# Performance work log

Measured on AMD Instinct MI355X. Metric: run time of the kernel, lower is better.

Reference implementation:

```python
import jax, jax.numpy as jnp
import numpy as np

NUM_ENTITIES = 600
FIRST_ENTITY = 0
LAST_ENTITY = 511  # inclusive, as in attentions[:, first:last+1]
EPS = 1e-9


def setup_inputs() -> dict:
    key = jax.random.key(0)
    k1, k2, k3, k4 = jax.random.split(key, 4)
    B, S, E = 64, 4096, 128
    doc_emb = jax.random.normal(k1, (B, S, E), dtype=jnp.float32)
    query_emb = jax.random.normal(k2, (B, E), dtype=jnp.float32)
    doc_ids = jax.random.randint(k3, (B, S), 0, NUM_ENTITIES, dtype=jnp.int32)
    seq_length = jax.random.randint(k4, (B,), 0, S, dtype=jnp.int32)
    return {"doc_emb": doc_emb, "query_emb": query_emb,
            "doc_ids": doc_ids, "seq_length": seq_length}


def reference(doc_emb, query_emb, doc_ids, seq_length):
    B, S, E = doc_emb.shape
    # --- _calculate_attention: batched mat-vec + length-masked softmax ---
    scores = jnp.einsum('bse,be->bs', doc_emb, query_emb)          # [B,S]
    seq_len = jnp.maximum(seq_length, 1)                            # guard empty docs
    valid = jnp.arange(S)[None, :] < seq_len[:, None]               # [B,S] bool
    scores = jnp.where(valid, scores, jnp.float32(-1e30))
    attentions = jax.nn.softmax(scores, axis=-1)                    # [B,S]
    # --- _sum_attentions: per-batch unsorted_segment_sum over entity ids ---
    # offset trick replaces tf.map_fn-serialized segment sums with one batched scatter
    seg_ids = (doc_ids + jnp.arange(B, dtype=doc_ids.dtype)[:, None] * NUM_ENTITIES).reshape(-1)
    sums = jax.ops.segment_sum(attentions.reshape(-1), seg_ids,
                               num_segments=B * NUM_ENTITIES)
    sums = sums.reshape(B, NUM_ENTITIES)[:, FIRST_ENTITY:LAST_ENTITY + 1]  # [B,512]
    # --- softmax_inverse: log (eps for numerical safety on zero-mass entities) ---
    logits = jnp.log(sums + EPS)
    return logits
```

## Files before the change

kernel.cpp:

```cpp
#include <hip/hip_runtime.h>
#include <hip/hip_bf16.h>
#include <math.h>

#define BB 64
#define SS 4096
#define EE 128
#define NENT 600
#define NOUT 512

__global__ __launch_bounds__(256) void scores_kernel(
    const float* __restrict__ doc_emb,
    const float* __restrict__ query_emb,
    float* __restrict__ scores) {
  const int b     = blockIdx.y;
  const int chunk = blockIdx.x;
  const int tid   = threadIdx.x;
  const int wave  = tid >> 6;
  const int lane  = tid & 63;
  const int half  = lane >> 5;
  const int sub   = lane & 31;

  const float4 q = ((const float4*)(query_emb + b * EE))[sub];

  const float* base = doc_emb + (size_t)b * SS * EE;
  const int s0 = chunk * 128 + wave * 2 + half;

#pragma unroll
  for (int it = 0; it < 16; ++it) {
    const int s = s0 + it * 8;
    const float4 d = ((const float4*)(base + (size_t)s * EE))[sub];
    float p = d.x * q.x + d.y * q.y + d.z * q.z + d.w * q.w;
#pragma unroll
    for (int off = 16; off; off >>= 1) p += __shfl_down(p, off, 32);
    if (sub == 0) scores[b * SS + s] = p;
  }
}

__global__ __launch_bounds__(1024) void finish_kernel(
    const float* __restrict__ scores,
    const int* __restrict__ doc_ids,
    const int* __restrict__ seq_length,
    float* __restrict__ out) {
  const int b   = blockIdx.x;
  const int tid = threadIdx.x;
  const int lane = tid & 63;
  const int wv   = tid >> 6;

  int len = seq_length[b];
  if (len < 1) len = 1;

  __shared__ float red[16];
  __shared__ float s_max, s_sum;
  __shared__ float bins[NENT];

  const float* sc = scores + b * SS;

  float vals[4];
  float lmax = -1e30f;
#pragma unroll
  for (int i = 0; i < 4; ++i) {
    const int s = tid + i * 1024;
    const float v = (s < len) ? sc[s] : -1e30f;
    vals[i] = v;
    lmax = fmaxf(lmax, v);
  }
#pragma unroll
  for (int off = 32; off; off >>= 1) lmax = fmaxf(lmax, __shfl_down(lmax, off, 64));
  if (lane == 0) red[wv] = lmax;
  __syncthreads();
  if (tid < 16) {
    float m = red[tid];
#pragma unroll
    for (int off = 8; off; off >>= 1) m = fmaxf(m, __shfl_down(m, off, 16));
    if (tid == 0) s_max = m;
  }
  __syncthreads();
  const float mx = s_max;
  __syncthreads();

  float lsum = 0.f;
#pragma unroll
  for (int i = 0; i < 4; ++i) {
    const int s = tid + i * 1024;
    const float e = (s < len) ? expf(vals[i] - mx) : 0.f;
    vals[i] = e;
    lsum += e;
  }
#pragma unroll
  for (int off = 32; off; off >>= 1) lsum += __shfl_down(lsum, off, 64);
  if (lane == 0) red[wv] = lsum;
  __syncthreads();
  if (tid < 16) {
    float m = red[tid];
#pragma unroll
    for (int off = 8; off; off >>= 1) m += __shfl_down(m, off, 16);
    if (tid == 0) s_sum = m;
  }
  for (int i = tid; i < NENT; i += 1024) bins[i] = 0.f;
  __syncthreads();
  const float inv = 1.f / s_sum;

  const int* ids = doc_ids + b * SS;
#pragma unroll
  for (int i = 0; i < 4; ++i) {
    const int s = tid + i * 1024;
    if (s < len) atomicAdd(&bins[ids[s]], vals[i] * inv);
  }
  __syncthreads();

  if (tid < NOUT) out[b * NOUT + tid] = logf(bins[tid] + 1e-9f);
}

extern "C" void kernel_launch(void* const* d_in, const int* in_sizes, int n_in,
                              void* d_out, int out_size, void* d_ws, size_t ws_size,
                              hipStream_t stream) {
  const float* doc_emb    = (const float*)d_in[0];
  const float* query_emb  = (const float*)d_in[1];
  const int*   doc_ids    = (const int*)d_in[2];
  const int*   seq_length = (const int*)d_in[3];
  float* out    = (float*)d_out;
  float* scores = (float*)d_ws;

  dim3 grid1(SS / 128, BB);
  scores_kernel<<<grid1, 256, 0, stream>>>(doc_emb, query_emb, scores);
  finish_kernel<<<BB, 1024, 0, stream>>>(scores, doc_ids, seq_length, out);
}
```

Baseline: 202.7 us.

## Fuse scoring, exponentiation and segment-sum via global atomics without max subtraction

Folds the softmax and segment-sum into the score kernel. Each score is exponentiated directly, with no max subtraction, and atomically added into global per-entity bins and a per-batch denominator. A small finalize kernel then normalizes and takes the log. This removes the scores round-trip and the single-block-per-batch finish kernel, but adds a memset, global atomic contention, and a risk of overflow or precision loss because exp is taken without the max shift.

```diff
diff --git a/kernel.cpp b/kernel.cpp
--- a/kernel.cpp
+++ b/kernel.cpp
@@ -8,10 +8,13 @@
 #define NENT 600
 #define NOUT 512
 
-__global__ __launch_bounds__(256) void scores_kernel(
+__global__ __launch_bounds__(256) void fused_kernel(
     const float* __restrict__ doc_emb,
     const float* __restrict__ query_emb,
-    float* __restrict__ scores) {
+    const int* __restrict__ doc_ids,
+    const int* __restrict__ seq_length,
+    float* __restrict__ bins,
+    float* __restrict__ denom) {
   const int b     = blockIdx.y;
   const int chunk = blockIdx.x;
   const int tid   = threadIdx.x;
@@ -20,10 +23,16 @@
   const int half  = lane >> 5;
   const int sub   = lane & 31;
 
+  int len = seq_length[b];
+  if (len < 1) len = 1;
+
   const float4 q = ((const float4*)(query_emb + b * EE))[sub];
+  const float* base = doc_emb + (size_t)b * SS * EE;
+  const int* ids = doc_ids + b * SS;
+  float* mybins = bins + b * NENT;
 
-  const float* base = doc_emb + (size_t)b * SS * EE;
   const int s0 = chunk * 128 + wave * 2 + half;
+  float dsum = 0.f;
 
 #pragma unroll
   for (int it = 0; it < 16; ++it) {
@@ -32,83 +41,24 @@
     float p = d.x * q.x + d.y * q.y + d.z * q.z + d.w * q.w;
 #pragma unroll
     for (int off = 16; off; off >>= 1) p += __shfl_down(p, off, 32);
-    if (sub == 0) scores[b * SS + s] = p;
+    if (sub == 0 && s < len) {
+      const float e = __expf(p);
+      atomicAdd(&mybins[ids[s]], e);
+      dsum += e;
+    }
   }
+  dsum += __shfl_down(dsum, 32, 64);
+  if (lane == 0 && dsum > 0.f) atomicAdd(&denom[b], dsum);
 }
 
-__global__ __launch_bounds__(1024) void finish_kernel(
-    const float* __restrict__ scores,
-    const int* __restrict__ doc_ids,
-    const int* __restrict__ seq_length,
+__global__ __launch_bounds__(512) void finalize_kernel(
+    const float* __restrict__ bins,
+    const float* __restrict__ denom,
     float* __restrict__ out) {
-  const int b   = blockIdx.x;
-  const int tid = threadIdx.x;
-  const int lane = tid & 63;
-  const int wv   = tid >> 6;
-
-  int len = seq_length[b];
-  if (len < 1) len = 1;
-
-  __shared__ float red[16];
-  __shared__ float s_max, s_sum;
-  __shared__ float bins[NENT];
-
-  const float* sc = scores + b * SS;
-
-  float vals[4];
-  float lmax = -1e30f;
-#pragma unroll
-  for (int i = 0; i < 4; ++i) {
-    const int s = tid + i * 1024;
-    const float v = (s < len) ? sc[s] : -1e30f;
-    vals[i] = v;
-    lmax = fmaxf(lmax, v);
-  }
-#pragma unroll
-  for (int off = 32; off; off >>= 1) lmax = fmaxf(lmax, __shfl_down(lmax, off, 64));
-  if (lane == 0) red[wv] = lmax;
-  __syncthreads();
-  if (tid < 16) {
-    float m = red[tid];
-#pragma unroll
-    for (int off = 8; off; off >>= 1) m = fmaxf(m, __shfl_down(m, off, 16));
-    if (tid == 0) s_max = m;
-  }
-  __syncthreads();
-  const float mx = s_max;
-  __syncthreads();
-
-  float lsum = 0.f;
-#pragma unroll
-  for (int i = 0; i < 4; ++i) {
-    const int s = tid + i * 1024;
-    const float e = (s < len) ? expf(vals[i] - mx) : 0.f;
-    vals[i] = e;
-    lsum += e;
-  }
-#pragma unroll
-  for (int off = 32; off; off >>= 1) lsum += __shfl_down(lsum, off, 64);
-  if (lane == 0) red[wv] = lsum;
-  __syncthreads();
-  if (tid < 16) {
-    float m = red[tid];
-#pragma unroll
-    for (int off = 8; off; off >>= 1) m += __shfl_down(m, off, 16);
-    if (tid == 0) s_sum = m;
-  }
-  for (int i = tid; i < NENT; i += 1024) bins[i] = 0.f;
-  __syncthreads();
-  const float inv = 1.f / s_sum;
-
-  const int* ids = doc_ids + b * SS;
-#pragma unroll
-  for (int i = 0; i < 4; ++i) {
-    const int s = tid + i * 1024;
-    if (s < len) atomicAdd(&bins[ids[s]], vals[i] * inv);
-  }
-  __syncthreads();
-
-  if (tid < NOUT) out[b * NOUT + tid] = logf(bins[tid] + 1e-9f);
+  const int b = blockIdx.x;
+  const float inv = 1.f / denom[b];
+  const int e = threadIdx.x;
+  out[b * NOUT + e] = logf(bins[b * NENT + e] * inv + 1e-9f);
 }
 
 extern "C" void kernel_launch(void* const* d_in, const int* in_sizes, int n_in,
@@ -118,10 +68,13 @@
   const float* query_emb  = (const float*)d_in[1];
   const int*   doc_ids    = (const int*)d_in[2];
   const int*   seq_length = (const int*)d_in[3];
-  float* out    = (float*)d_out;
-  float* scores = (float*)d_ws;
+  float* out   = (float*)d_out;
+  float* bins  = (float*)d_ws;
+  float* denom = bins + BB * NENT;
 
-  dim3 grid1(SS / 128, BB);
-  scores_kernel<<<grid1, 256, 0, stream>>>(doc_emb, query_emb, scores);
-  finish_kernel<<<BB, 1024, 0, stream>>>(scores, doc_ids, seq_length, out);
+  hipMemsetAsync(d_ws, 0, (size_t)(BB * NENT + BB) * sizeof(float), stream);
+
+  fused_kernel<<<dim3(SS / 128, BB), 256, 0, stream>>>(
+      doc_emb, query_emb, doc_ids, seq_length, bins, denom);
+  finalize_kernel<<<BB, NOUT, 0, stream>>>(bins, denom, out);
 }
```

Measured after the change: 221.1 us. 1.09x slower.
